# Optimization experiments

Measured on AMD Instinct MI355X. Metric: run time of the kernel, lower is better.

Reference implementation:

```python
import jax, jax.numpy as jnp
import numpy as np

D_MODEL = 1024
NUM_HEADS = 16
WINDOW = 2048  # must equal seq_len (see notes): source matmul attn(B,H,S,W) @ v(B,H,S,hd) requires W == S
SEQ_LEN = 2048
BATCH = 1


def setup_inputs() -> dict:
    key = jax.random.key(0)
    k0, k1, k2 = jax.random.split(key, 3)
    d = D_MODEL
    x = jax.random.normal(k0, (BATCH, SEQ_LEN, d), dtype=jnp.float32)
    w_qkv = jax.random.normal(k1, (3 * d, d), dtype=jnp.float32) * (d ** -0.5)
    b_qkv = jnp.zeros((3 * d,), dtype=jnp.float32)
    w_proj = jax.random.normal(k2, (d, d), dtype=jnp.float32) * (d ** -0.5)
    b_proj = jnp.zeros((d,), dtype=jnp.float32)
    return {"x": x, "w_qkv": w_qkv, "b_qkv": b_qkv, "w_proj": w_proj, "b_proj": b_proj}


def reference(x, w_qkv, b_qkv, w_proj, b_proj):
    B, S, d = x.shape
    H = NUM_HEADS
    hd = d // H
    W = WINDOW
    scale = hd ** -0.5

    # qkv projection (torch Linear: x @ W^T + b)
    qkv = x @ w_qkv.T + b_qkv                      # (B, S, 3d)
    qkv = qkv.reshape(B, S, 3, H, hd).transpose(2, 0, 3, 1, 4)  # (3, B, H, S, hd)
    q, k, v = qkv[0], qkv[1], qkv[2]

    # sliding-window scores: score[b,h,i,j] = q_i . k_padded[i+j] * scale, j in [0, W)
    pad = W // 2
    k_pad = jnp.pad(k, ((0, 0), (0, 0), (pad, pad), (0, 0)))     # (B, H, S+W, hd)
    scores_full = jnp.einsum('bhid,bhjd->bhij', q, k_pad) * scale  # (B, H, S, S+W)
    idx = jnp.arange(S)[:, None] + jnp.arange(W)[None, :]          # (S, W) banded gather indices
    scores = jnp.take_along_axis(scores_full, idx[None, None], axis=-1)  # (B, H, S, W)

    attn = jax.nn.softmax(scores, axis=-1)
    attn = jnp.nan_to_num(attn)  # faithful to torch.nan_to_num(attn, 0.0)

    # Faithful to the source: forward() does matmul(attn, v), i.e. column j of the
    # windowed attn indexes v position j directly (requires W == S).
    out = jnp.einsum('bhij,bhjd->bhid', attn, v)   # (B, H, S, hd)
    out = out.transpose(0, 2, 1, 3).reshape(B, S, d)
    out = out @ w_proj.T + b_proj
    return out, attn
```

## Files before the change

kernel.cpp:

```cpp
#include <hip/hip_runtime.h>
#include <hip/hip_bf16.h>

typedef __hip_bfloat16 bf16;
typedef __attribute__((ext_vector_type(8))) short short8;
typedef __attribute__((ext_vector_type(4))) float f32x4;

#define DEV static __device__ __forceinline__

static constexpr int SEQ = 2048;
static constexpr int DM  = 1024;
static constexpr int NH  = 16;
static constexpr int HD  = 64;
static constexpr int WIN = 2048;
static constexpr int PAD = 1024;

DEV void async16(const void* g, void* l) {
  __builtin_amdgcn_global_load_lds(
      (__attribute__((address_space(1))) void*)(g),
      (__attribute__((address_space(3))) void*)(l), 16, 0, 0);
}

__global__ __launch_bounds__(256) void k_cvt(const float* __restrict__ x,
                                             const float* __restrict__ wq,
                                             const float* __restrict__ wp,
                                             bf16* __restrict__ xb,
                                             bf16* __restrict__ wqb,
                                             bf16* __restrict__ wpb) {
  const int NX = SEQ * DM, NQ = 3 * DM * DM, NP = DM * DM;
  const int tot = (NX + NQ + NP) >> 2;
  const int stride = gridDim.x * 256;
  for (int i = blockIdx.x * 256 + threadIdx.x; i < tot; i += stride) {
    int e = i << 2;
    const float* s; bf16* d; int o;
    if (e < NX)            { s = x;  d = xb;  o = e; }
    else if (e < NX + NQ)  { s = wq; d = wqb; o = e - NX; }
    else                   { s = wp; d = wpb; o = e - NX - NQ; }
    float4 v = *(const float4*)(s + o);
    __align__(8) bf16 t4[4] = {__float2bfloat16(v.x), __float2bfloat16(v.y),
                               __float2bfloat16(v.z), __float2bfloat16(v.w)};
    *(uint2*)(d + o) = *(uint2*)t4;
  }
}

DEV void gemm_core(const bf16* __restrict__ A, const bf16* __restrict__ B,
                   int m0, int n0, int K, int tid, bf16* As, bf16* Bs,
                   f32x4 (&acc)[4][4]) {
  const int lane = tid & 63, wid = tid >> 6;
  const int wm = wid >> 1, wn = wid & 1;
  const int l15 = lane & 15, l4 = lane >> 4;
  for (int k0 = 0; k0 < K; k0 += 64) {
    __syncthreads();
    #pragma unroll
    for (int it = 0; it < 4; ++it) {
      int rb = it * 32 + wid * 8;
      int r  = rb + (lane >> 3);
      int c  = (lane & 7) * 8;
      async16(A + (size_t)(m0 + r) * K + k0 + c, As + rb * 64);
      async16(B + (size_t)(n0 + r) * K + k0 + c, Bs + rb * 64);
    }
    asm volatile("s_waitcnt vmcnt(0)" ::: "memory");
    __syncthreads();
    #pragma unroll
    for (int kk = 0; kk < 2; ++kk) {
      short8 a[4], b[4];
      #pragma unroll
      for (int im = 0; im < 4; ++im)
        a[im] = *(const short8*)(As + (wm * 64 + im * 16 + l15) * 64 + kk * 32 + l4 * 8);
      #pragma unroll
      for (int in = 0; in < 4; ++in)
        b[in] = *(const short8*)(Bs + (wn * 64 + in * 16 + l15) * 64 + kk * 32 + l4 * 8);
      #pragma unroll
      for (int im = 0; im < 4; ++im)
        #pragma unroll
        for (int in = 0; in < 4; ++in)
          acc[im][in] = __builtin_amdgcn_mfma_f32_16x16x32_bf16(a[im], b[in], acc[im][in], 0, 0, 0);
    }
  }
}

__global__ __launch_bounds__(256) void k_gemm_qkv(const bf16* __restrict__ A,
                                                  const bf16* __restrict__ B,
                                                  const float* __restrict__ bias,
                                                  bf16* __restrict__ qo,
                                                  bf16* __restrict__ ko,
                                                  bf16* __restrict__ vt) {
  __shared__ bf16 As[128 * 64], Bs[128 * 64];
  const int tid = threadIdx.x, lane = tid & 63;
  const int wid = tid >> 6, wm = wid >> 1, wn = wid & 1;
  const int l15 = lane & 15, l4 = lane >> 4;
  const int m0 = blockIdx.x * 128, n0 = blockIdx.y * 128;
  f32x4 acc[4][4] = {};
  gemm_core(A, B, m0, n0, DM, tid, As, Bs, acc);
  #pragma unroll
  for (int im = 0; im < 4; ++im)
    #pragma unroll
    for (int in = 0; in < 4; ++in) {
      int col = n0 + wn * 64 + in * 16 + l15;
      float bval = bias[col];
      int t = col >> 10, h = (col >> 6) & 15, dd = col & 63;
      int row0 = m0 + wm * 64 + im * 16 + l4 * 4;
      if (t == 2) {
        __align__(8) bf16 t4[4];
        #pragma unroll
        for (int r = 0; r < 4; ++r)
          t4[r] = __float2bfloat16(acc[im][in][r] + bval);
        *(uint2*)&vt[((size_t)h * HD + dd) * SEQ + row0] = *(uint2*)t4;
      } else {
        #pragma unroll
        for (int r = 0; r < 4; ++r) {
          float v = acc[im][in][r] + bval;
          size_t idx = ((size_t)h * SEQ + row0 + r) * HD + dd;
          if (t == 0) qo[idx] = __float2bfloat16(v * 0.18033688011112042f);
          else        ko[idx] = __float2bfloat16(v);
        }
      }
    }
}

DEV void stage_kp(const bf16* kbase, int i0, int tt, int lane, bf16* dst) {
  #pragma unroll
  for (int it = 0; it < 4; ++it) {
    int r  = it * 8 + (lane >> 3);
    int cg = lane & 7;
    int jp = i0 + tt * 32 + r;
    int krow = jp - PAD;
    krow = krow < 0 ? 0 : (krow > SEQ - 1 ? SEQ - 1 : krow);
    int sc = (cg ^ (r & 7)) * 8;
    async16(kbase + (size_t)krow * HD + sc, dst + it * 8 * 64);
  }
}

DEV void qk_mfma_lds(const bf16* KPb, const short8 (&qf)[2][2], int l15, int l4,
                     f32x4 (&sf)[2][2]) {
  __builtin_amdgcn_s_setprio(1);
  #pragma unroll
  for (int kg = 0; kg < 2; ++kg) {
    short8 kfr[2];
    #pragma unroll
    for (int fn = 0; fn < 2; ++fn) {
      int jl = fn * 16 + l15;
      int pg = (kg * 4 + l4) ^ (jl & 7);
      kfr[fn] = *(const short8*)&KPb[jl * 64 + pg * 8];
    }
    #pragma unroll
    for (int fm = 0; fm < 2; ++fm)
      #pragma unroll
      for (int fn = 0; fn < 2; ++fn)
        sf[fm][fn] = __builtin_amdgcn_mfma_f32_16x16x32_bf16(qf[fm][kg], kfr[fn], sf[fm][fn], 0, 0, 0);
  }
  __builtin_amdgcn_s_setprio(0);
}

DEV void qk_mfma_lds_sw(const bf16* KPb, const short8 (&qf)[2][2], int l15, int l4,
                        f32x4 (&sf)[2][2]) {
  __builtin_amdgcn_s_setprio(1);
  #pragma unroll
  for (int kg = 0; kg < 2; ++kg) {
    short8 kfr[2];
    #pragma unroll
    for (int fj = 0; fj < 2; ++fj) {
      int jl = fj * 16 + l15;
      int pg = (kg * 4 + l4) ^ (jl & 7);
      kfr[fj] = *(const short8*)&KPb[jl * 64 + pg * 8];
    }
    #pragma unroll
    for (int fj = 0; fj < 2; ++fj)
      #pragma unroll
      for (int fi = 0; fi < 2; ++fi)
        sf[fj][fi] = __builtin_amdgcn_mfma_f32_16x16x32_bf16(kfr[fj], qf[fi][kg], sf[fj][fi], 0, 0, 0);
  }
  __builtin_amdgcn_s_setprio(0);
}

DEV int pad_lo(int i0) { int d = PAD - i0; return d <= 0 ? 0 : (d >> 5); }
DEV int pad_hi(int i0) { int t = ((PAD + SEQ - 1 - i0) >> 5) + 1; return t > 65 ? 65 : t; }

__global__ __launch_bounds__(256) void k_attn1(const bf16* __restrict__ q,
                                               const bf16* __restrict__ kkk,
                                               float* __restrict__ psums,
                                               float* __restrict__ aof) {
  const int h  = blockIdx.x >> 6;
  const int i0 = (blockIdx.x & 63) << 5;
  const int tid = threadIdx.x;
  const int c = tid >> 6;
  const int lane = tid & 63;
  const int l15 = lane & 15, l4 = lane >> 4;

  __shared__ bf16 KP[4][2][32 * 64];

  {
    f32x4 z = {0.f, 0.f, 0.f, 0.f};
    size_t zb = ((size_t)h * SEQ + i0) * (HD / 4);
    ((f32x4*)aof)[zb + tid]       = z;
    ((f32x4*)aof)[zb + 256 + tid] = z;
  }

  constexpr int st[5] = {0, 16, 32, 48, 65};
  const int lo_g = pad_lo(i0), hi_g = pad_hi(i0);
  int lo = st[c] > lo_g ? st[c] : lo_g;
  int hi = st[c + 1] < hi_g ? st[c + 1] : hi_g;

  short8 qf[2][2];
  #pragma unroll
  for (int fi = 0; fi < 2; ++fi)
    #pragma unroll
    for (int kg = 0; kg < 2; ++kg)
      qf[fi][kg] = *(const short8*)&q[((size_t)h * SEQ + i0 + fi * 16 + l15) * HD + kg * 32 + l4 * 8];

  const bf16* kbase = kkk + (size_t)h * SEQ * HD;

  float psum[2] = {0.f, 0.f};
  if (lo < hi) {
    stage_kp(kbase, i0, lo, lane, KP[c][lo & 1]);
    for (int tt = lo; tt < hi; ++tt) {
      int nxt = (tt + 1 < hi) ? tt + 1 : tt;
      stage_kp(kbase, i0, nxt, lane, KP[c][(tt + 1) & 1]);
      asm volatile("s_waitcnt vmcnt(4)" ::: "memory");
      f32x4 sf[2][2] = {};
      qk_mfma_lds_sw(KP[c][tt & 1], qf, l15, l4, sf);
      const bool interior = (tt >= 1) && (tt <= 63) &&
                            (i0 + tt * 32 >= PAD) && (i0 + tt * 32 + 31 < PAD + SEQ);
      if (interior) {
        #pragma unroll
        for (int fj = 0; fj < 2; ++fj)
          #pragma unroll
          for (int r = 0; r < 4; ++r) {
            psum[0] += __builtin_amdgcn_exp2f(sf[fj][0][r]);
            psum[1] += __builtin_amdgcn_exp2f(sf[fj][1][r]);
          }
      } else {
        #pragma unroll
        for (int fj = 0; fj < 2; ++fj)
          #pragma unroll
          for (int r = 0; r < 4; ++r) {
            int jj = tt * 32 + fj * 16 + l4 * 4 + r;
            int jp = i0 + jj;
            bool pad = (jp < PAD) || (jp >= PAD + SEQ);
            #pragma unroll
            for (int fi = 0; fi < 2; ++fi) {
              int iloc = fi * 16 + l15;
              float e = pad ? 1.0f : __builtin_amdgcn_exp2f(sf[fj][fi][r]);
              if ((unsigned)(jj - iloc) < (unsigned)WIN) psum[fi] += e;
            }
          }
      }
    }
  }
  float r0 = psum[0];
  r0 += __shfl_xor(r0, 16); r0 += __shfl_xor(r0, 32);
  float r1 = psum[1];
  r1 += __shfl_xor(r1, 16); r1 += __shfl_xor(r1, 32);
  if (lane < 32) {
    int i_abs = i0 + lane;
    float s = (lane < 16) ? r0 : r1;
    if (c == 0) {
      int cl = i0 + lo_g * 32 - i_abs; if (cl < 0) cl = 0;
      int cr = i_abs + WIN - (i0 + hi_g * 32); if (cr < 0) cr = 0;
      s += (float)(cl + cr);
    }
    psums[((size_t)c * NH + h) * SEQ + i_abs] = s;
  }
}

__global__ __launch_bounds__(256) void k_attn2(const bf16* __restrict__ q,
                                               const bf16* __restrict__ kkk,
                                               const bf16* __restrict__ vT,
                                               const float* __restrict__ psums,
                                               float* __restrict__ attn,
                                               float* __restrict__ aof) {
  const int h  = blockIdx.x >> 6;
  const int i0 = (blockIdx.x & 63) << 5;
  const int tid = threadIdx.x;
  const int c = tid >> 6;
  const int lane = tid & 63;
  const int l15 = lane & 15, l4 = lane >> 4;
  const int c0 = c * 16, c1 = c0 + 16;
  const int lo_g = pad_lo(i0), hi_g = pad_hi(i0);

  __shared__ bf16 KP[4][2][32 * 64];
  __shared__ float JF[4][32 * 64];

  float inv[2][4];
  #pragma unroll
  for (int fm = 0; fm < 2; ++fm)
    #pragma unroll
    for (int r = 0; r < 4; ++r) {
      int row = i0 + fm * 16 + l4 * 4 + r;
      float s = 0.f;
      #pragma unroll
      for (int cc = 0; cc < 4; ++cc)
        s += psums[((size_t)cc * NH + h) * SEQ + row];
      inv[fm][r] = __builtin_amdgcn_rcpf(s);
    }

  short8 qf[2][2];
  #pragma unroll
  for (int fm = 0; fm < 2; ++fm)
    #pragma unroll
    for (int kg = 0; kg < 2; ++kg)
      qf[fm][kg] = *(const short8*)&q[((size_t)h * SEQ + i0 + fm * 16 + l15) * HD + kg * 32 + l4 * 8];

  const bf16* kbase = kkk + (size_t)h * SEQ * HD;
  const bf16* vbase = vT + (size_t)h * HD * SEQ;
  float* abase = attn + (size_t)(h * SEQ + i0) * WIN;
  float* JFW = JF[c];

  f32x4 oacc[2][4] = {};
  stage_kp(kbase, i0, c0, lane, KP[c][0]);
  for (int tt = c0; tt <= c1; ++tt) {
    short8 bv[4];
    if (tt > c0) {
      int jb = (tt - 1) * 32;
      #pragma unroll
      for (int nd = 0; nd < 4; ++nd)
        bv[nd] = *(const short8*)&vbase[(size_t)(nd * 16 + l15) * SEQ + jb + l4 * 8];
    }
    int nxt = (tt < c1) ? tt + 1 : tt;
    stage_kp(kbase, i0, nxt, lane, KP[c][(tt + 1) & 1]);
    if (tt == c0)          asm volatile("s_waitcnt vmcnt(4)" ::: "memory");
    else if (tt == c0 + 1) asm volatile("s_waitcnt vmcnt(8)" ::: "memory");
    else                   asm volatile("s_waitcnt vmcnt(12)" ::: "memory");

    const bool fp = (tt < lo_g) || (tt >= hi_g);
    f32x4 sf[2][2] = {};
    if (!fp) qk_mfma_lds(KP[c][tt & 1], qf, l15, l4, sf);

    const bool allv = (i0 + tt * 32 >= PAD) && (i0 + tt * 32 + 31 < PAD + SEQ);
    #pragma unroll
    for (int fm = 0; fm < 2; ++fm)
      #pragma unroll
      for (int fn = 0; fn < 2; ++fn) {
        int J0 = tt * 32 + fn * 16 + l15;
        bool padc = fp || (!allv && ((i0 + J0 < PAD) || (i0 + J0 >= PAD + SEQ)));
        #pragma unroll
        for (int r = 0; r < 4; ++r) {
          int row = fm * 16 + l4 * 4 + r;
          float e = padc ? 1.0f : __builtin_amdgcn_exp2f(sf[fm][fn][r]);
          float val = e * inv[fm][r];
          int j6 = (J0 - row) & 63;
          int pgrp = (j6 >> 2) ^ ((row & 7) << 1);
          JFW[row * 64 + pgrp * 4 + (j6 & 3)] = val;
        }
      }

    if (tt > c0) {
      const int g = (tt - 1) & 1;
      const int Jb = (tt - 1) * 32;
      #pragma unroll
      for (int s = 0; s < 4; ++s) {
        int row = s * 8 + (lane >> 3);
        int c8 = lane & 7;
        int pgrp = (g * 8 + c8) ^ ((row & 7) << 1);
        f32x4 vv = *(const f32x4*)&JFW[row * 64 + pgrp * 4];
        __builtin_nontemporal_store(vv, (f32x4*)(abase + (size_t)row * WIN + Jb + c8 * 4));
      }
      short8 af[2];
      #pragma unroll
      for (int fm = 0; fm < 2; ++fm) {
        int row = fm * 16 + l15;
        int pg0 = (g * 8 + l4 * 2) ^ ((row & 7) << 1);
        const float* p = &JFW[row * 64 + pg0 * 4];
        union { unsigned short u[8]; short8 v; } tmp;
        #pragma unroll
        for (int e = 0; e < 8; ++e)
          tmp.u[e] = __bfloat16_as_ushort(__float2bfloat16(p[e]));
        af[fm] = tmp.v;
      }
      __builtin_amdgcn_s_setprio(1);
      #pragma unroll
      for (int fm = 0; fm < 2; ++fm)
        #pragma unroll
        for (int nd = 0; nd < 4; ++nd)
          oacc[fm][nd] = __builtin_amdgcn_mfma_f32_16x16x32_bf16(af[fm], bv[nd], oacc[fm][nd], 0, 0, 0);
      __builtin_amdgcn_s_setprio(0);
    }
  }
  #pragma unroll
  for (int fm = 0; fm < 2; ++fm)
    #pragma unroll
    for (int nd = 0; nd < 4; ++nd)
      #pragma unroll
      for (int r = 0; r < 4; ++r) {
        int i  = i0 + fm * 16 + l4 * 4 + r;
        int dd = nd * 16 + l15;
        atomicAdd(&aof[((size_t)h * SEQ + i) * HD + dd], oacc[fm][nd][r]);
      }
}

__global__ __launch_bounds__(256) void k_ored(const float* __restrict__ aof,
                                              bf16* __restrict__ ao) {
  int f = blockIdx.x * 256 + threadIdx.x;
  int e = f << 2;
  int h  = e >> 17;
  int i  = (e >> 6) & (SEQ - 1);
  int dd = e & 63;
  float4 v = ((const float4*)aof)[f];
  __align__(8) bf16 t4[4] = {__float2bfloat16(v.x), __float2bfloat16(v.y),
                             __float2bfloat16(v.z), __float2bfloat16(v.w)};
  *(uint2*)&ao[(size_t)i * DM + h * HD + dd] = *(uint2*)t4;
}

__global__ __launch_bounds__(256) void k_gemm_proj(const bf16* __restrict__ A,
                                                   const bf16* __restrict__ B,
                                                   const float* __restrict__ bias,
                                                   float* __restrict__ out) {
  __shared__ bf16 As[128 * 64], Bs[128 * 64];
  const int tid = threadIdx.x, lane = tid & 63;
  const int wid = tid >> 6, wm = wid >> 1, wn = wid & 1;
  const int l15 = lane & 15, l4 = lane >> 4;
  const int m0 = blockIdx.x * 128, n0 = blockIdx.y * 128;
  f32x4 acc[4][4] = {};
  gemm_core(A, B, m0, n0, DM, tid, As, Bs, acc);
  #pragma unroll
  for (int im = 0; im < 4; ++im)
    #pragma unroll
    for (int in = 0; in < 4; ++in) {
      int col = n0 + wn * 64 + in * 16 + l15;
      float bval = bias[col];
      #pragma unroll
      for (int r = 0; r < 4; ++r) {
        int row = m0 + wm * 64 + im * 16 + l4 * 4 + r;
        out[(size_t)row * DM + col] = acc[im][in][r] + bval;
      }
    }
}

extern "C" void kernel_launch(void* const* d_in, const int* in_sizes, int n_in,
                              void* d_out, int out_size, void* d_ws, size_t ws_size,
                              hipStream_t stream) {
  (void)in_sizes; (void)n_in; (void)out_size; (void)ws_size;
  const float* x  = (const float*)d_in[0];
  const float* wq = (const float*)d_in[1];
  const float* bq = (const float*)d_in[2];
  const float* wp = (const float*)d_in[3];
  const float* bp = (const float*)d_in[4];
  float* out  = (float*)d_out;
  float* attn = out + (size_t)SEQ * DM;

  char* ws = (char*)d_ws;
  bf16* xb    = (bf16*)(ws + (size_t) 0);
  bf16* wqb   = (bf16*)(ws + ((size_t)4  << 20));
  bf16* wpb   = (bf16*)(ws + ((size_t)10 << 20));
  bf16* qarr  = (bf16*)(ws + ((size_t)12 << 20));
  bf16* karr  = (bf16*)(ws + ((size_t)16 << 20));
  bf16* vt    = (bf16*)(ws + ((size_t)24 << 20));
  bf16* ao    = (bf16*)(ws + ((size_t)28 << 20));
  float* aof  = (float*)(ws + (size_t)0);
  float* psums= (float*)(ws + ((size_t)8 << 20));

  k_cvt<<<dim3(1024), dim3(256), 0, stream>>>(x, wq, wp, xb, wqb, wpb);
  k_gemm_qkv<<<dim3(16, 24), dim3(256), 0, stream>>>(xb, wqb, bq, qarr, karr, vt);
  k_attn1<<<dim3(1024), dim3(256), 0, stream>>>(qarr, karr, psums, aof);
  k_attn2<<<dim3(1024), dim3(256), 0, stream>>>(qarr, karr, vt, psums, attn, aof);
  k_ored<<<dim3(NH * SEQ * HD / 4 / 256), dim3(256), 0, stream>>>(aof, ao);
  k_gemm_proj<<<dim3(16, 8), dim3(256), 0, stream>>>(ao, wpb, bp, out);
}
```

Before: 162.6 us.

## Fuse attention passes into one kernel with register-cached exponentials

Merges the row-sum pass, the normalize/PV pass and the output reduction into a single attention kernel. Each wave computes QK^T and exp once, caches the exponentials packed as bf16 in registers, reduces row sums across waves through shared memory, and then normalizes and runs the PV MFMAs. The global atomics and the separate reduction kernel are replaced by an in-block shared-memory sum that writes bf16 output directly. This removes the duplicated QK^T/exp work and two kernel launches. In exchange it adds heavy register pressure (a 17x8 packed array per lane) and rounds the exponentials to bf16 before normalization, which may affect the precision of the attention output.

```diff
diff --git a/kernel.cpp b/kernel.cpp
--- a/kernel.cpp
+++ b/kernel.cpp
@@ -151,147 +151,28 @@
   __builtin_amdgcn_s_setprio(0);
 }
 
-DEV void qk_mfma_lds_sw(const bf16* KPb, const short8 (&qf)[2][2], int l15, int l4,
-                        f32x4 (&sf)[2][2]) {
-  __builtin_amdgcn_s_setprio(1);
-  #pragma unroll
-  for (int kg = 0; kg < 2; ++kg) {
-    short8 kfr[2];
-    #pragma unroll
-    for (int fj = 0; fj < 2; ++fj) {
-      int jl = fj * 16 + l15;
-      int pg = (kg * 4 + l4) ^ (jl & 7);
-      kfr[fj] = *(const short8*)&KPb[jl * 64 + pg * 8];
-    }
-    #pragma unroll
-    for (int fj = 0; fj < 2; ++fj)
-      #pragma unroll
-      for (int fi = 0; fi < 2; ++fi)
-        sf[fj][fi] = __builtin_amdgcn_mfma_f32_16x16x32_bf16(kfr[fj], qf[fi][kg], sf[fj][fi], 0, 0, 0);
-  }
-  __builtin_amdgcn_s_setprio(0);
-}
-
 DEV int pad_lo(int i0) { int d = PAD - i0; return d <= 0 ? 0 : (d >> 5); }
 DEV int pad_hi(int i0) { int t = ((PAD + SEQ - 1 - i0) >> 5) + 1; return t > 65 ? 65 : t; }
 
-__global__ __launch_bounds__(256) void k_attn1(const bf16* __restrict__ q,
-                                               const bf16* __restrict__ kkk,
-                                               float* __restrict__ psums,
-                                               float* __restrict__ aof) {
+__global__ __launch_bounds__(256, 2) void k_attn(const bf16* __restrict__ q,
+                                                 const bf16* __restrict__ kkk,
+                                                 const bf16* __restrict__ vT,
+                                                 float* __restrict__ attn,
+                                                 bf16* __restrict__ ao) {
   const int h  = blockIdx.x >> 6;
   const int i0 = (blockIdx.x & 63) << 5;
   const int tid = threadIdx.x;
   const int c = tid >> 6;
   const int lane = tid & 63;
   const int l15 = lane & 15, l4 = lane >> 4;
-
-  __shared__ bf16 KP[4][2][32 * 64];
-
-  {
-    f32x4 z = {0.f, 0.f, 0.f, 0.f};
-    size_t zb = ((size_t)h * SEQ + i0) * (HD / 4);
-    ((f32x4*)aof)[zb + tid]       = z;
-    ((f32x4*)aof)[zb + 256 + tid] = z;
-  }
-
-  constexpr int st[5] = {0, 16, 32, 48, 65};
+  const int c0 = c * 16;
   const int lo_g = pad_lo(i0), hi_g = pad_hi(i0);
-  int lo = st[c] > lo_g ? st[c] : lo_g;
-  int hi = st[c + 1] < hi_g ? st[c + 1] : hi_g;
-
-  short8 qf[2][2];
-  #pragma unroll
-  for (int fi = 0; fi < 2; ++fi)
-    #pragma unroll
-    for (int kg = 0; kg < 2; ++kg)
-      qf[fi][kg] = *(const short8*)&q[((size_t)h * SEQ + i0 + fi * 16 + l15) * HD + kg * 32 + l4 * 8];
-
-  const bf16* kbase = kkk + (size_t)h * SEQ * HD;
-
-  float psum[2] = {0.f, 0.f};
-  if (lo < hi) {
-    stage_kp(kbase, i0, lo, lane, KP[c][lo & 1]);
-    for (int tt = lo; tt < hi; ++tt) {
-      int nxt = (tt + 1 < hi) ? tt + 1 : tt;
-      stage_kp(kbase, i0, nxt, lane, KP[c][(tt + 1) & 1]);
-      asm volatile("s_waitcnt vmcnt(4)" ::: "memory");
-      f32x4 sf[2][2] = {};
-      qk_mfma_lds_sw(KP[c][tt & 1], qf, l15, l4, sf);
-      const bool interior = (tt >= 1) && (tt <= 63) &&
-                            (i0 + tt * 32 >= PAD) && (i0 + tt * 32 + 31 < PAD + SEQ);
-      if (interior) {
-        #pragma unroll
-        for (int fj = 0; fj < 2; ++fj)
-          #pragma unroll
-          for (int r = 0; r < 4; ++r) {
-            psum[0] += __builtin_amdgcn_exp2f(sf[fj][0][r]);
-            psum[1] += __builtin_amdgcn_exp2f(sf[fj][1][r]);
-          }
-      } else {
-        #pragma unroll
-        for (int fj = 0; fj < 2; ++fj)
-          #pragma unroll
-          for (int r = 0; r < 4; ++r) {
-            int jj = tt * 32 + fj * 16 + l4 * 4 + r;
-            int jp = i0 + jj;
-            bool pad = (jp < PAD) || (jp >= PAD + SEQ);
-            #pragma unroll
-            for (int fi = 0; fi < 2; ++fi) {
-              int iloc = fi * 16 + l15;
-              float e = pad ? 1.0f : __builtin_amdgcn_exp2f(sf[fj][fi][r]);
-              if ((unsigned)(jj - iloc) < (unsigned)WIN) psum[fi] += e;
-            }
-          }
-      }
-    }
-  }
-  float r0 = psum[0];
-  r0 += __shfl_xor(r0, 16); r0 += __shfl_xor(r0, 32);
-  float r1 = psum[1];
-  r1 += __shfl_xor(r1, 16); r1 += __shfl_xor(r1, 32);
-  if (lane < 32) {
-    int i_abs = i0 + lane;
-    float s = (lane < 16) ? r0 : r1;
-    if (c == 0) {
-      int cl = i0 + lo_g * 32 - i_abs; if (cl < 0) cl = 0;
-      int cr = i_abs + WIN - (i0 + hi_g * 32); if (cr < 0) cr = 0;
-      s += (float)(cl + cr);
-    }
-    psums[((size_t)c * NH + h) * SEQ + i_abs] = s;
-  }
-}
-
-__global__ __launch_bounds__(256) void k_attn2(const bf16* __restrict__ q,
-                                               const bf16* __restrict__ kkk,
-                                               const bf16* __restrict__ vT,
-                                               const float* __restrict__ psums,
-                                               float* __restrict__ attn,
-                                               float* __restrict__ aof) {
-  const int h  = blockIdx.x >> 6;
-  const int i0 = (blockIdx.x & 63) << 5;
-  const int tid = threadIdx.x;
-  const int c = tid >> 6;
-  const int lane = tid & 63;
-  const int l15 = lane & 15, l4 = lane >> 4;
-  const int c0 = c * 16, c1 = c0 + 16;
-  const int lo_g = pad_lo(i0), hi_g = pad_hi(i0);
-
-  __shared__ bf16 KP[4][2][32 * 64];
-  __shared__ float JF[4][32 * 64];
-
-  float inv[2][4];
-  #pragma unroll
-  for (int fm = 0; fm < 2; ++fm)
-    #pragma unroll
-    for (int r = 0; r < 4; ++r) {
-      int row = i0 + fm * 16 + l4 * 4 + r;
-      float s = 0.f;
-      #pragma unroll
-      for (int cc = 0; cc < 4; ++cc)
-        s += psums[((size_t)cc * NH + h) * SEQ + row];
-      inv[fm][r] = __builtin_amdgcn_rcpf(s);
-    }
+
+  __shared__ __align__(16) char Ubuf[32 * 1024];
+  __shared__ float sums[4][32];
+  bf16*  KP0 = (bf16*)Ubuf + (c * 2 + 0) * 2048;
+  bf16*  KP1 = (bf16*)Ubuf + (c * 2 + 1) * 2048;
+  float* JFW = (float*)Ubuf + c * 2048;
 
   short8 qf[2][2];
   #pragma unroll
@@ -303,52 +184,114 @@
   const bf16* kbase = kkk + (size_t)h * SEQ * HD;
   const bf16* vbase = vT + (size_t)h * HD * SEQ;
   float* abase = attn + (size_t)(h * SEQ + i0) * WIN;
-  float* JFW = JF[c];
+
+  unsigned int ep[17][2][2][2];
+  float psum[2][4] = {};
+
+  stage_kp(kbase, i0, c0, lane, KP0);
+  #pragma unroll
+  for (int s = 0; s < 17; ++s) {
+    const int tt = c0 + s;
+    int nxt = (s < 16) ? tt + 1 : tt;
+    stage_kp(kbase, i0, nxt, lane, ((tt + 1) & 1) ? KP1 : KP0);
+    asm volatile("s_waitcnt vmcnt(4)" ::: "memory");
+
+    const bool fp = (tt < lo_g) || (tt >= hi_g);
+    f32x4 sf[2][2] = {};
+    if (!fp) qk_mfma_lds((tt & 1) ? KP1 : KP0, qf, l15, l4, sf);
+
+    const bool allv = (i0 + tt * 32 >= PAD) && (i0 + tt * 32 + 31 < PAD + SEQ);
+    #pragma unroll
+    for (int fm = 0; fm < 2; ++fm)
+      #pragma unroll
+      for (int fn = 0; fn < 2; ++fn) {
+        const int J0 = tt * 32 + fn * 16 + l15;
+        const bool padc = fp || (!allv && ((i0 + J0 < PAD) || (i0 + J0 >= PAD + SEQ)));
+        #pragma unroll
+        for (int p = 0; p < 2; ++p) {
+          float e0 = padc ? 1.0f : __builtin_amdgcn_exp2f(sf[fm][fn][2 * p]);
+          float e1 = padc ? 1.0f : __builtin_amdgcn_exp2f(sf[fm][fn][2 * p + 1]);
+          unsigned lo16 = __bfloat16_as_ushort(__float2bfloat16(e0));
+          unsigned hi16 = __bfloat16_as_ushort(__float2bfloat16(e1));
+          ep[s][fm][fn][p] = lo16 | (hi16 << 16);
+          if (s < 16) {
+            if (s == 0 && c == 0) {
+              int iloc = fm * 16 + l4 * 4 + 2 * p;
+              int j0v = J0 - iloc;
+              if ((unsigned)j0v < (unsigned)WIN) psum[fm][2 * p] += e0;
+              if ((unsigned)(j0v - 1) < (unsigned)WIN) psum[fm][2 * p + 1] += e1;
+            } else {
+              psum[fm][2 * p] += e0;
+              psum[fm][2 * p + 1] += e1;
+            }
+          } else if (c == 3) {
+            int iloc = fm * 16 + l4 * 4 + 2 * p;
+            int j0v = J0 - iloc;
+            if ((unsigned)j0v < (unsigned)WIN) psum[fm][2 * p] += e0;
+            if ((unsigned)(j0v - 1) < (unsigned)WIN) psum[fm][2 * p + 1] += e1;
+          }
+        }
+      }
+  }
+
+  #pragma unroll
+  for (int fm = 0; fm < 2; ++fm)
+    #pragma unroll
+    for (int r = 0; r < 4; ++r) {
+      float s = psum[fm][r];
+      s += __shfl_xor(s, 1); s += __shfl_xor(s, 2);
+      s += __shfl_xor(s, 4); s += __shfl_xor(s, 8);
+      if (l15 == 0) sums[c][fm * 16 + l4 * 4 + r] = s;
+    }
+  __syncthreads();
+
+  float inv[2][4];
+  #pragma unroll
+  for (int fm = 0; fm < 2; ++fm)
+    #pragma unroll
+    for (int r = 0; r < 4; ++r) {
+      int row = fm * 16 + l4 * 4 + r;
+      inv[fm][r] = __builtin_amdgcn_rcpf(sums[0][row] + sums[1][row] +
+                                         sums[2][row] + sums[3][row]);
+    }
 
   f32x4 oacc[2][4] = {};
-  stage_kp(kbase, i0, c0, lane, KP[c][0]);
-  for (int tt = c0; tt <= c1; ++tt) {
+  #pragma unroll
+  for (int s = 0; s < 17; ++s) {
+    const int tt = c0 + s;
     short8 bv[4];
-    if (tt > c0) {
+    if (s > 0) {
       int jb = (tt - 1) * 32;
       #pragma unroll
       for (int nd = 0; nd < 4; ++nd)
         bv[nd] = *(const short8*)&vbase[(size_t)(nd * 16 + l15) * SEQ + jb + l4 * 8];
     }
-    int nxt = (tt < c1) ? tt + 1 : tt;
-    stage_kp(kbase, i0, nxt, lane, KP[c][(tt + 1) & 1]);
-    if (tt == c0)          asm volatile("s_waitcnt vmcnt(4)" ::: "memory");
-    else if (tt == c0 + 1) asm volatile("s_waitcnt vmcnt(8)" ::: "memory");
-    else                   asm volatile("s_waitcnt vmcnt(12)" ::: "memory");
-
-    const bool fp = (tt < lo_g) || (tt >= hi_g);
-    f32x4 sf[2][2] = {};
-    if (!fp) qk_mfma_lds(KP[c][tt & 1], qf, l15, l4, sf);
-
-    const bool allv = (i0 + tt * 32 >= PAD) && (i0 + tt * 32 + 31 < PAD + SEQ);
     #pragma unroll
     for (int fm = 0; fm < 2; ++fm)
       #pragma unroll
       for (int fn = 0; fn < 2; ++fn) {
-        int J0 = tt * 32 + fn * 16 + l15;
-        bool padc = fp || (!allv && ((i0 + J0 < PAD) || (i0 + J0 >= PAD + SEQ)));
-        #pragma unroll
-        for (int r = 0; r < 4; ++r) {
-          int row = fm * 16 + l4 * 4 + r;
-          float e = padc ? 1.0f : __builtin_amdgcn_exp2f(sf[fm][fn][r]);
-          float val = e * inv[fm][r];
-          int j6 = (J0 - row) & 63;
-          int pgrp = (j6 >> 2) ^ ((row & 7) << 1);
-          JFW[row * 64 + pgrp * 4 + (j6 & 3)] = val;
+        const int J0 = tt * 32 + fn * 16 + l15;
+        #pragma unroll
+        for (int p = 0; p < 2; ++p) {
+          unsigned u = ep[s][fm][fn][p];
+          float v0 = __uint_as_float(u << 16)          * inv[fm][2 * p];
+          float v1 = __uint_as_float(u & 0xffff0000u)  * inv[fm][2 * p + 1];
+          int row0 = fm * 16 + l4 * 4 + 2 * p;
+          int j60 = (J0 - row0) & 63;
+          int pg0 = (j60 >> 2) ^ ((row0 & 7) << 1);
+          JFW[row0 * 64 + pg0 * 4 + (j60 & 3)] = v0;
+          int row1 = row0 + 1;
+          int j61 = (J0 - row1) & 63;
+          int pg1 = (j61 >> 2) ^ ((row1 & 7) << 1);
+          JFW[row1 * 64 + pg1 * 4 + (j61 & 3)] = v1;
         }
       }
-
-    if (tt > c0) {
+    if (s > 0) {
       const int g = (tt - 1) & 1;
       const int Jb = (tt - 1) * 32;
       #pragma unroll
-      for (int s = 0; s < 4; ++s) {
-        int row = s * 8 + (lane >> 3);
+      for (int st = 0; st < 4; ++st) {
+        int row = st * 8 + (lane >> 3);
         int c8 = lane & 7;
         int pgrp = (g * 8 + c8) ^ ((row & 7) << 1);
         f32x4 vv = *(const f32x4*)&JFW[row * 64 + pgrp * 4];
@@ -375,29 +318,28 @@
       __builtin_amdgcn_s_setprio(0);
     }
   }
+
   #pragma unroll
   for (int fm = 0; fm < 2; ++fm)
     #pragma unroll
     for (int nd = 0; nd < 4; ++nd)
       #pragma unroll
-      for (int r = 0; r < 4; ++r) {
-        int i  = i0 + fm * 16 + l4 * 4 + r;
-        int dd = nd * 16 + l15;
-        atomicAdd(&aof[((size_t)h * SEQ + i) * HD + dd], oacc[fm][nd][r]);
-      }
-}
-
-__global__ __launch_bounds__(256) void k_ored(const float* __restrict__ aof,
-                                              bf16* __restrict__ ao) {
-  int f = blockIdx.x * 256 + threadIdx.x;
-  int e = f << 2;
-  int h  = e >> 17;
-  int i  = (e >> 6) & (SEQ - 1);
-  int dd = e & 63;
-  float4 v = ((const float4*)aof)[f];
-  __align__(8) bf16 t4[4] = {__float2bfloat16(v.x), __float2bfloat16(v.y),
-                             __float2bfloat16(v.z), __float2bfloat16(v.w)};
-  *(uint2*)&ao[(size_t)i * DM + h * HD + dd] = *(uint2*)t4;
+      for (int r = 0; r < 4; ++r)
+        JFW[(fm * 16 + l4 * 4 + r) * 64 + nd * 16 + l15] = oacc[fm][nd][r];
+  __syncthreads();
+  {
+    int row = tid >> 3;
+    int d0 = (tid & 7) * 8;
+    const float* j0p = (const float*)Ubuf;
+    union { unsigned short u[8]; short8 v; } o;
+    #pragma unroll
+    for (int e = 0; e < 8; ++e) {
+      int idx = row * 64 + d0 + e;
+      float s = j0p[idx] + j0p[2048 + idx] + j0p[4096 + idx] + j0p[6144 + idx];
+      o.u[e] = __bfloat16_as_ushort(__float2bfloat16(s));
+    }
+    *(short8*)&ao[(size_t)(i0 + row) * DM + h * HD + d0] = o.v;
+  }
 }
 
 __global__ __launch_bounds__(256) void k_gemm_proj(const bf16* __restrict__ A,
@@ -445,13 +387,9 @@
   bf16* karr  = (bf16*)(ws + ((size_t)16 << 20));
   bf16* vt    = (bf16*)(ws + ((size_t)24 << 20));
   bf16* ao    = (bf16*)(ws + ((size_t)28 << 20));
-  float* aof  = (float*)(ws + (size_t)0);
-  float* psums= (float*)(ws + ((size_t)8 << 20));
 
   k_cvt<<<dim3(1024), dim3(256), 0, stream>>>(x, wq, wp, xb, wqb, wpb);
   k_gemm_qkv<<<dim3(16, 24), dim3(256), 0, stream>>>(xb, wqb, bq, qarr, karr, vt);
-  k_attn1<<<dim3(1024), dim3(256), 0, stream>>>(qarr, karr, psums, aof);
-  k_attn2<<<dim3(1024), dim3(256), 0, stream>>>(qarr, karr, vt, psums, attn, aof);
-  k_ored<<<dim3(NH * SEQ * HD / 4 / 256), dim3(256), 0, stream>>>(aof, ao);
+  k_attn<<<dim3(1024), dim3(256), 0, stream>>>(qarr, karr, vt, attn, ao);
   k_gemm_proj<<<dim3(16, 8), dim3(256), 0, stream>>>(ao, wpb, bp, out);
 }
```

Result: slower. 304.7 us (+87.3%).
